# Performance work log

Measured on AMD Instinct MI355X. Metric: run time of the kernel, lower is better.

Reference implementation:

```python
import jax, jax.numpy as jnp
import numpy as np

# --- static configuration (matches init_kwargs / input_specs) ---
B, QB, D, NH, HD = 4, 512, 256, 8, 32   # batch, queries/batch, d_model, heads, head_dim
HALF = HD // 2                            # rotation pairs per head
L = 4                                     # n_levels
SIZES = [3, 5, 7, 9]                      # neighborhood size per level
K = sum(s * s for s in SIZES)             # 164 keys per query
SHAPES = np.array([[8, 8], [16, 16], [32, 32], [64, 64]], dtype=np.int32)
HMAX = 64                                 # finest-level spatial extent
LN_EPS = 1e-5
ROPE_THETA = 10.0


def make_rope_freqs():
    # Grouped-frequency ND RoPE: spatial dims (i, j) in freq group 0 (theta=10),
    # level dim in group 1 (theta = rope_theta/100 = 0.1). HALF slots split:
    # group0 -> HALF/2 (HALF/4 per spatial dim), group1 -> HALF/2.
    n_sp = HALF // 4   # 4 slots for i, 4 for j
    n_lv = HALF // 2   # 8 slots for level
    f = np.zeros((3, HALF), np.float32)
    f_sp = ROPE_THETA ** (-np.arange(n_sp, dtype=np.float32) / n_sp)
    f_lv = (ROPE_THETA / 100.0) ** (-np.arange(n_lv, dtype=np.float32) / n_lv)
    f[0, 0:n_sp] = f_sp
    f[1, n_sp:2 * n_sp] = f_sp
    f[2, 2 * n_sp:] = f_lv
    return jnp.asarray(np.tile(f[None], (NH, 1, 1)))  # [NH, 3, HALF]


def neighborhood_indices(qpos, shapes):
    # qpos: [N,4] float (b, i, j, level); queries live at the finest level so
    # (i, j) are full-scale coords. Returns (b,i,j,l) int indices [N,K,4] and
    # full-scale key positions (i_full, j_full, level) [N,K,3].
    N = qpos.shape[0]
    b = qpos[:, 0].astype(jnp.int32)
    q_ij = qpos[:, 1:3]
    shapes_f = shapes.astype(jnp.float32)
    scal = shapes_f / shapes_f[-1]  # [L,2]: H_l / H_finest
    idx_parts, pos_parts = [], []
    for m, size in enumerate(SIZES):
        center = jnp.floor(q_ij * scal[m]).astype(jnp.int32)  # [N,2] at level m
        r = jnp.arange(size, dtype=jnp.int32) - (size - 1) // 2
        off = jnp.stack(jnp.meshgrid(r, r, indexing='ij'), -1).reshape(-1, 2)
        nb = center[:, None, :] + off[None]                    # [N, s*s, 2]
        lev_i = jnp.full((N, size * size, 1), m, jnp.int32)
        idx_parts.append(jnp.concatenate([nb, lev_i], -1))
        pos_parts.append(jnp.concatenate(
            [nb.astype(jnp.float32) / scal[m],                 # back to full scale
             jnp.full((N, size * size, 1), float(m))], -1))
    ijl = jnp.concatenate(idx_parts, 1)       # [N,K,3]
    key_pos = jnp.concatenate(pos_parts, 1)   # [N,K,3]
    bijl = jnp.concatenate([jnp.broadcast_to(b[:, None, None], (N, K, 1)), ijl], -1)
    return bijl, key_pos


def gather_values(fmap, bijl, shapes):
    # fmap: dense stand-in for the sparse COO pyramid, [B, HMAX, HMAX, L, D];
    # level l only occupies the top-left [H_l, W_l] block -> out-of-range keys
    # are "unspecified" (value 0, masked out of the softmax).
    b, i, j, l = bijl[..., 0], bijl[..., 1], bijl[..., 2], bijl[..., 3]
    hw = shapes[l]  # [N,K,2]
    valid = (i >= 0) & (i < hw[..., 0]) & (j >= 0) & (j < hw[..., 1])
    ic = jnp.clip(i, 0, HMAX - 1)
    jc = jnp.clip(j, 0, HMAX - 1)
    val = fmap[b, ic, jc, l]  # [N,K,D]
    return val * valid[..., None], valid


def layer_norm(x, g, b_):
    mu = x.mean(-1, keepdims=True)
    var = ((x - mu) ** 2).mean(-1, keepdims=True)
    return (x - mu) * jax.lax.rsqrt(var + LN_EPS) * g + b_


def apply_rope(x, pos, freqs):
    # x: [..., NH, HD], pos: [..., 3], freqs: [NH, 3, HALF]
    ang = jnp.einsum('...p,hpf->...hf', pos, freqs)
    c, s = jnp.cos(ang), jnp.sin(ang)
    xr = x.reshape(x.shape[:-1] + (HALF, 2))
    x1, x2 = xr[..., 0], xr[..., 1]
    return jnp.stack([x1 * c - x2 * s, x1 * s + x2 * c], -1).reshape(x.shape)


def setup_inputs() -> dict:
    key = jax.random.key(0)
    ks = jax.random.split(key, 8)
    N = B * QB
    q_ij = jax.random.uniform(ks[0], (N, 2), minval=0.5, maxval=float(HMAX) - 0.5)
    batch = jnp.repeat(jnp.arange(B, dtype=jnp.float32), QB)
    lev = jnp.full((N, 1), float(L - 1))  # all queries at the finest level
    query_positions_bijl = jnp.concatenate([batch[:, None], q_ij, lev], -1)
    sc = D ** -0.5
    return {
        'query': jax.random.normal(ks[1], (N, D), jnp.float32),
        'query_positions_bijl': query_positions_bijl,
        'query_batch_offsets': jnp.arange(B + 1, dtype=jnp.int32) * QB,
        'stacked_feature_maps': jax.random.normal(ks[2], (B, HMAX, HMAX, L, D), jnp.float32),
        'level_spatial_shapes': jnp.asarray(SHAPES),
        'ln_gamma': jnp.ones((D,), jnp.float32),
        'ln_beta': jnp.zeros((D,), jnp.float32),
        'Wq': jax.random.normal(ks[3], (D, D), jnp.float32) * sc,
        'Wkv': jax.random.normal(ks[4], (D, 2 * D), jnp.float32) * sc,
        'Wout': jax.random.normal(ks[5], (D, D), jnp.float32) * sc,
        'rope_freqs': make_rope_freqs(),
    }


def reference(query, query_positions_bijl, query_batch_offsets, stacked_feature_maps,
              level_spatial_shapes, ln_gamma, ln_beta, Wq, Wkv, Wout, rope_freqs):
    N = query.shape[0]
    bijl, key_pos = neighborhood_indices(query_positions_bijl, level_spatial_shapes)
    value, specified = gather_values(stacked_feature_maps, bijl, level_spatial_shapes)
    residual = query
    qn = layer_norm(query, ln_gamma, ln_beta)  # norm_first
    q = qn @ Wq                                # [N, D]
    kv = value @ Wkv                           # [N, K, 2D]
    k, v = jnp.split(kv, 2, axis=-1)
    q = apply_rope(q.reshape(B, QB, NH, HD),
                   query_positions_bijl[:, 1:].reshape(B, QB, 3), rope_freqs)
    k = apply_rope(k.reshape(B, QB, K, NH, HD),
                   key_pos.reshape(B, QB, K, 3), rope_freqs)
    v = v.reshape(B, QB, K, NH, HD)
    # NOTE: original module applies no 1/sqrt(head_dim) scaling -- kept faithful.
    scores = jnp.einsum('bqhd,bqkhd->bhqk', q, k)
    mask = specified.reshape(B, QB, K)[:, None]  # [B,1,QB,K]
    scores = jnp.where(mask, scores, -jnp.inf)
    w = jax.nn.softmax(scores, axis=-1)
    x = jnp.einsum('bhqk,bqkhd->bqhd', w, v)
    x = x.reshape(N, D) @ Wout
    return x + residual
```

## Files before the change

### kernel.cpp

```cpp
#include <hip/hip_runtime.h>
#include <math.h>

#define NQ    2048
#define Dd    256
#define NHh   8
#define HDd   32
#define KK    164
#define KP    192
#define PPB   5440
#define M_TOT 21760
#define TWO_D 512

using bf16x8  = __attribute__((ext_vector_type(8))) short;
using f32x4   = __attribute__((ext_vector_type(4))) float;
using ushort8 = __attribute__((ext_vector_type(8))) unsigned short;

__device__ __forceinline__ unsigned short bf16_rne(float x) {
    unsigned u = __float_as_uint(x);
    return (unsigned short)((u + 0x7fffu + ((u >> 16) & 1u)) >> 16);
}
__device__ __forceinline__ float bf2f(unsigned short h) {
    return __uint_as_float((unsigned)h << 16);
}

__device__ __forceinline__ void gload_lds16(const void* g, void* s) {
    __builtin_amdgcn_global_load_lds(
        (const __attribute__((address_space(1))) void*)g,
        (__attribute__((address_space(3))) void*)s, 16, 0, 0);
}

__device__ __forceinline__ void row_geom(int r, int& l, int& S, int& base, int& lg, int& inv) {
    if      (r < 64)   { l = 0; S = 8;  base = 0;    lg = 3; inv = 8; }
    else if (r < 320)  { l = 1; S = 16; base = 64;   lg = 4; inv = 4; }
    else if (r < 1344) { l = 2; S = 32; base = 320;  lg = 5; inv = 2; }
    else               { l = 3; S = 64; base = 1344; lg = 6; inv = 1; }
}

__device__ __forceinline__ void split_one(const float* __restrict__ W,
                                          unsigned short* __restrict__ hi_,
                                          unsigned short* __restrict__ lo_,
                                          int N, int gid) {
    int k = gid & 255, n = gid >> 8;
    float x = W[k * N + n];
    unsigned short h = bf16_rne(x);
    hi_[n * 256 + k] = h;
    lo_[n * 256 + k] = bf16_rne(x - bf2f(h));
}

__global__ __launch_bounds__(256) void prep(const float* __restrict__ fmap,
                                            const float* __restrict__ Wkv,
                                            const float* __restrict__ Wq,
                                            const float* __restrict__ Wout,
                                            const float* __restrict__ query,
                                            const float* __restrict__ gamma,
                                            const float* __restrict__ beta,
                                            unsigned short* __restrict__ Ahi,
                                            unsigned short* __restrict__ Alo,
                                            unsigned short* __restrict__ WkvThi,
                                            unsigned short* __restrict__ WkvTlo,
                                            unsigned short* __restrict__ WqThi,
                                            unsigned short* __restrict__ WqTlo,
                                            unsigned short* __restrict__ WoThi,
                                            unsigned short* __restrict__ WoTlo,
                                            unsigned short* __restrict__ Xhi,
                                            unsigned short* __restrict__ Xlo) {
    __shared__ float red[4];
    const int bid = blockIdx.x, t = threadIdx.x;

    if (bid < 5440) {
        int gid = bid * 256 + t;
        int m = gid >> 6, c4 = (gid & 63) << 2;
        int b = m / PPB, r = m - b * PPB;
        int l, S, base, lg, inv;
        row_geom(r, l, S, base, lg, inv);
        int idx = r - base;
        int i = idx >> lg, j = idx & (S - 1);
        size_t rowOff = ((size_t)((b * 64 + i) * 64 + j)) * 1024 + l * 256;
        const float4 v = *(const float4*)(fmap + rowOff + c4);
        ushort4 hi, lo;
        hi.x = bf16_rne(v.x); lo.x = bf16_rne(v.x - bf2f(hi.x));
        hi.y = bf16_rne(v.y); lo.y = bf16_rne(v.y - bf2f(hi.y));
        hi.z = bf16_rne(v.z); lo.z = bf16_rne(v.z - bf2f(hi.z));
        hi.w = bf16_rne(v.w); lo.w = bf16_rne(v.w - bf2f(hi.w));
        *(ushort4*)(Ahi + (size_t)m * 256 + c4) = hi;
        *(ushort4*)(Alo + (size_t)m * 256 + c4) = lo;
    } else if (bid < 5952) {
        split_one(Wkv, WkvThi, WkvTlo, 512, (bid - 5440) * 256 + t);
    } else if (bid < 6208) {
        split_one(Wq, WqThi, WqTlo, 256, (bid - 5952) * 256 + t);
    } else if (bid < 6464) {
        split_one(Wout, WoThi, WoTlo, 256, (bid - 6208) * 256 + t);
    } else {
        const int q = bid - 6464, wid = t >> 6;
        float x = query[q * Dd + t];
        float s = x;
#pragma unroll
        for (int mK = 32; mK >= 1; mK >>= 1) s += __shfl_xor(s, mK);
        if ((t & 63) == 0) red[wid] = s;
        __syncthreads();
        float mu = (red[0] + red[1] + red[2] + red[3]) * (1.0f / 256.0f);
        float dx = x - mu;
        float s2 = dx * dx;
#pragma unroll
        for (int mK = 32; mK >= 1; mK >>= 1) s2 += __shfl_xor(s2, mK);
        __syncthreads();
        if ((t & 63) == 0) red[wid] = s2;
        __syncthreads();
        float var = (red[0] + red[1] + red[2] + red[3]) * (1.0f / 256.0f);
        float v = dx * rsqrtf(var + 1e-5f) * gamma[t] + beta[t];
        unsigned short hi = bf16_rne(v);
        Xhi[q * Dd + t] = hi;
        Xlo[q * Dd + t] = bf16_rne(v - bf2f(hi));
    }
}

__global__ __launch_bounds__(256) void kv_gemm_mfma(const unsigned short* __restrict__ Ahi,
                                                    const unsigned short* __restrict__ Alo,
                                                    const unsigned short* __restrict__ Bthi,
                                                    const unsigned short* __restrict__ Btlo,
                                                    const float* __restrict__ freqs,
                                                    unsigned short* __restrict__ kv16) {
    __shared__ __align__(16) short As[2][2][128 * 32];
    __shared__ __align__(16) short Bs[2][2][128 * 32];

    const int bid = blockIdx.x;
    const int my = (bid >> 5) * 8 + (bid & 7);
    const int mx = (bid >> 3) & 3;
    if (my >= 170) return;

    const int t  = threadIdx.x;
    const int w  = t >> 6, l = t & 63;
    const int wr = w >> 1, wc = w & 1;
    const int n0 = mx * 128, bm = my * 128;
    const int lr = l & 15, ks = l >> 4;
    const int ksw8 = ((ks ^ ((lr >> 1) & 3)) << 3);
    const bool doRope = (n0 < 256);

    f32x4 acc[4][4];
#pragma unroll
    for (int i = 0; i < 4; i++)
#pragma unroll
        for (int j = 0; j < 4; j++) { f32x4 z = {0.f,0.f,0.f,0.f}; acc[i][j] = z; }

    const int srow = l >> 2, sslot = l & 3;
    const int gs = sslot ^ ((srow >> 1) & 3);

    auto stage = [&](int kt, int buf) {
        size_t k0b = (size_t)(kt << 6);
#pragma unroll
        for (int i = 0; i < 2; i++) {
            int rb = w * 32 + i * 16;
            int m  = rb + srow;
            size_t aofs = (((size_t)(bm + m)) << 9) + k0b + (gs << 4);
            size_t bofs = (((size_t)(n0 + m)) << 9) + k0b + (gs << 4);
            gload_lds16((const char*)Ahi  + aofs, (void*)&As[buf][0][rb * 32]);
            gload_lds16((const char*)Alo  + aofs, (void*)&As[buf][1][rb * 32]);
            gload_lds16((const char*)Bthi + bofs, (void*)&Bs[buf][0][rb * 32]);
            gload_lds16((const char*)Btlo + bofs, (void*)&Bs[buf][1][rb * 32]);
        }
    };

    stage(0, 0);
    __syncthreads();

    for (int kt = 0; kt < 8; kt++) {
        int cur = kt & 1;
        if (kt < 7) stage(kt + 1, cur ^ 1);

        bf16x8 aH[4], aL[4], bH[4], bL[4];
#pragma unroll
        for (int f = 0; f < 4; f++) {
            int m = wr * 64 + f * 16 + lr;
            aH[f] = *(const bf16x8*)&As[cur][0][m * 32 + ksw8];
            aL[f] = *(const bf16x8*)&As[cur][1][m * 32 + ksw8];
            int n = wc * 64 + f * 16 + lr;
            bH[f] = *(const bf16x8*)&Bs[cur][0][n * 32 + ksw8];
            bL[f] = *(const bf16x8*)&Bs[cur][1][n * 32 + ksw8];
        }
#pragma unroll
        for (int i = 0; i < 4; i++)
#pragma unroll
            for (int j = 0; j < 4; j++)
                acc[i][j] = __builtin_amdgcn_mfma_f32_16x16x32_bf16(aH[i], bH[j],
                                                                    acc[i][j], 0, 0, 0);
#pragma unroll
        for (int i = 0; i < 4; i++)
#pragma unroll
            for (int j = 0; j < 4; j++)
                acc[i][j] = __builtin_amdgcn_mfma_f32_16x16x32_bf16(aH[i], bL[j],
                                                                    acc[i][j], 0, 0, 0);
#pragma unroll
        for (int i = 0; i < 4; i++)
#pragma unroll
            for (int j = 0; j < 4; j++)
                acc[i][j] = __builtin_amdgcn_mfma_f32_16x16x32_bf16(aL[i], bH[j],
                                                                    acc[i][j], 0, 0, 0);
        __syncthreads();
    }

    float fx0 = 0.f, fy0 = 0.f, fz0 = 0.f, fx1 = 0.f, fy1 = 0.f, fz1 = 0.f;
    if (doRope) {
        int e0 = lr >> 1, e1 = e0 + 8;
        fx0 = freqs[e0]; fy0 = freqs[16 + e0]; fz0 = freqs[32 + e0];
        fx1 = freqs[e1]; fy1 = freqs[16 + e1]; fz1 = freqs[32 + e1];
    }
#pragma unroll
    for (int i = 0; i < 4; i++) {
        int mg = bm + wr * 64 + i * 16 + ks * 4;
#pragma unroll
        for (int r = 0; r < 4; r++) {
            int m = mg + r;
            float c0 = 1.f, s0 = 0.f, c1 = 1.f, s1 = 0.f;
            if (doRope) {
                int b = m / PPB;
                int rw = m - b * PPB;
                int lL, S, base, lg, inv;
                row_geom(rw, lL, S, base, lg, inv);
                int idx = rw - base;
                float px = (float)((idx >> lg) * inv);
                float py = (float)((idx & (S - 1)) * inv);
                float pl = (float)lL;
                __sincosf(px * fx0 + py * fy0 + pl * fz0, &s0, &c0);
                __sincosf(px * fx1 + py * fy1 + pl * fz1, &s1, &c1);
            }
#pragma unroll
            for (int j = 0; j < 4; j++) {
                int ng = n0 + wc * 64 + j * 16 + lr;
                float self = acc[i][j][r];
                float part = __shfl_xor(self, 1);
                if (!(lr & 1)) {
                    float y1 = self, y2 = part;
                    if (doRope) {
                        float c = (j & 1) ? c1 : c0;
                        float s = (j & 1) ? s1 : s0;
                        y1 = self * c - part * s;
                        y2 = self * s + part * c;
                    }
                    unsigned word = (unsigned)bf16_rne(y1) | ((unsigned)bf16_rne(y2) << 16);
                    *(unsigned*)(kv16 + (size_t)m * TWO_D + ng) = word;
                }
            }
        }
    }
}

template<bool RESID>
__global__ __launch_bounds__(256) void proj_gemm(const unsigned short* __restrict__ Ahi,
                                                 const unsigned short* __restrict__ Alo,
                                                 const unsigned short* __restrict__ Bthi,
                                                 const unsigned short* __restrict__ Btlo,
                                                 float* __restrict__ C,
                                                 const float* __restrict__ resid) {
    __shared__ __align__(16) short As[2][2][64 * 32];
    __shared__ __align__(16) short Bs[2][2][32 * 32];

    const int t  = threadIdx.x;
    const int w  = t >> 6, l = t & 63;
    const int n0 = blockIdx.x * 32, bm = blockIdx.y * 64;
    const int lr = l & 15, ks = l >> 4;
    const int ksw8 = ((ks ^ ((lr >> 1) & 3)) << 3);

    f32x4 acc[2];
#pragma unroll
    for (int j = 0; j < 2; j++) { f32x4 z = {0.f,0.f,0.f,0.f}; acc[j] = z; }

    const int srow = l >> 2, sslot = l & 3;
    const int gs = sslot ^ ((srow >> 1) & 3);

    auto stage = [&](int kt, int buf) {
        size_t k0b = (size_t)(kt << 6);
        {
            int rb = w * 16;
            int m  = rb + srow;
            size_t aofs = (((size_t)(bm + m)) << 9) + k0b + (gs << 4);
            gload_lds16((const char*)Ahi + aofs, (void*)&As[buf][0][rb * 32]);
            gload_lds16((const char*)Alo + aofs, (void*)&As[buf][1][rb * 32]);
        }
        {
            int sel = w >> 1;
            int rb  = (w & 1) * 16;
            int m   = rb + srow;
            const unsigned short* Bp = sel ? Btlo : Bthi;
            size_t bofs = (((size_t)(n0 + m)) << 9) + k0b + (gs << 4);
            gload_lds16((const char*)Bp + bofs, (void*)&Bs[buf][sel][rb * 32]);
        }
    };

    stage(0, 0);
    __syncthreads();

    for (int kt = 0; kt < 8; kt++) {
        int cur = kt & 1;
        if (kt < 7) stage(kt + 1, cur ^ 1);

        bf16x8 aH, aL, bH[2], bL[2];
        {
            int m = w * 16 + lr;
            aH = *(const bf16x8*)&As[cur][0][m * 32 + ksw8];
            aL = *(const bf16x8*)&As[cur][1][m * 32 + ksw8];
        }
#pragma unroll
        for (int j = 0; j < 2; j++) {
            int n = j * 16 + lr;
            bH[j] = *(const bf16x8*)&Bs[cur][0][n * 32 + ksw8];
            bL[j] = *(const bf16x8*)&Bs[cur][1][n * 32 + ksw8];
        }
#pragma unroll
        for (int j = 0; j < 2; j++)
            acc[j] = __builtin_amdgcn_mfma_f32_16x16x32_bf16(aH, bH[j], acc[j], 0, 0, 0);
#pragma unroll
        for (int j = 0; j < 2; j++)
            acc[j] = __builtin_amdgcn_mfma_f32_16x16x32_bf16(aH, bL[j], acc[j], 0, 0, 0);
#pragma unroll
        for (int j = 0; j < 2; j++)
            acc[j] = __builtin_amdgcn_mfma_f32_16x16x32_bf16(aL, bH[j], acc[j], 0, 0, 0);
        __syncthreads();
    }

    {
        int mg = bm + w * 16 + ks * 4;
#pragma unroll
        for (int j = 0; j < 2; j++) {
            int ng = n0 + j * 16 + lr;
#pragma unroll
            for (int r = 0; r < 4; r++) {
                float v = acc[j][r];
                if (RESID) v += resid[(size_t)(mg + r) * 256 + ng];
                C[(size_t)(mg + r) * 256 + ng] = v;
            }
        }
    }
}

__global__ __launch_bounds__(256) void attn_core(const float* __restrict__ qr,
                                                 const float* __restrict__ qpos,
                                                 const unsigned short* __restrict__ kv16,
                                                 const float* __restrict__ freqs,
                                                 unsigned short* __restrict__ Phi,
                                                 unsigned short* __restrict__ Plo) {
    __shared__ __align__(16) float qsh[Dd];
    __shared__ float sL[NHh * KP];
    __shared__ int   kidx[KP];
    __shared__ float attnP[8][Dd];
    __shared__ float invS[NHh];

    const int q = ((blockIdx.x & 7) << 8) | (blockIdx.x >> 3);
    const int t = threadIdx.x;
    const int h = t >> 5, lane = t & 31;

    float qx = qpos[q * 4 + 1];
    float qy = qpos[q * 4 + 2];
    int   bb = (int)qpos[q * 4 + 0];

    {
        float x = qr[q * Dd + t];
        int f = (t & 31) >> 1;
        float ang = qx * freqs[f] + qy * freqs[16 + f] + 3.0f * freqs[32 + f];
        float c = cosf(ang), sn = sinf(ang);
        float partner = __shfl_xor(x, 1);
        qsh[t] = (!(t & 1)) ? (x * c - partner * sn) : (partner * sn + x * c);
    }

    if (t < KP) {
        int k = t;
        int kv = -1;
        if (k < KK) {
            int S, base, off, sz, half, lg;
            if      (k < 9)  { S = 8;  base = 0;    off = k;      sz = 3; half = 1; lg = 3; }
            else if (k < 34) { S = 16; base = 64;   off = k - 9;  sz = 5; half = 2; lg = 4; }
            else if (k < 83) { S = 32; base = 320;  off = k - 34; sz = 7; half = 3; lg = 5; }
            else             { S = 64; base = 1344; off = k - 83; sz = 9; half = 4; lg = 6; }
            int di = off / sz - half;
            int dj = off % sz - half;
            float scal = (float)S * (1.0f / 64.0f);
            int ci = (int)floorf(qx * scal);
            int cj = (int)floorf(qy * scal);
            int i = ci + di, j = cj + dj;
            bool valid = (i >= 0) & (i < S) & (j >= 0) & (j < S);
            kv = valid ? (bb * PPB + base + (i << lg) + j) : -1;
        }
        kidx[t] = kv;
    }
    __syncthreads();

    float qreg[32];
#pragma unroll
    for (int i = 0; i < 32; i++) qreg[i] = qsh[h * HDd + i];

#pragma unroll
    for (int ct = 0; ct < 6; ++ct) {
        int k = ct * 32 + lane;
        int ki = kidx[k];
        int kr = ki < 0 ? 0 : ki;
        const ushort8* kp = (const ushort8*)(kv16 + (size_t)kr * TWO_D + h * HDd);
        float c0 = 0.f, c1 = 0.f;
#pragma unroll
        for (int s4 = 0; s4 < 4; s4++) {
            ushort8 kvv = kp[s4];
            float* cc = (s4 & 1) ? &c1 : &c0;
#pragma unroll
            for (int e = 0; e < 8; e++)
                *cc = fmaf(qreg[s4 * 8 + e], bf2f(kvv[e]), *cc);
        }
        sL[h * KP + k] = (ki >= 0) ? (c0 + c1) : -INFINITY;
    }
    __syncthreads();

    float mx = -INFINITY;
#pragma unroll
    for (int ct = 0; ct < 6; ++ct) mx = fmaxf(mx, sL[h * KP + ct * 32 + lane]);
#pragma unroll
    for (int mK = 16; mK >= 1; mK >>= 1) mx = fmaxf(mx, __shfl_xor(mx, mK));
    float se = 0.f;
#pragma unroll
    for (int ct = 0; ct < 6; ++ct) {
        int k = ct * 32 + lane;
        float e = __expf(sL[h * KP + k] - mx);
        sL[h * KP + k] = e;
        se += e;
    }
#pragma unroll
    for (int mK = 16; mK >= 1; mK >>= 1) se += __shfl_xor(se, mK);
    if (lane == 0) invS[h] = 1.0f / se;
    __syncthreads();

    {
        const int rep  = t >> 6;
        const int half = (t >> 5) & 1;
        const int l5   = t & 31;
        const int hh   = l5 >> 2;
        const int oct  = l5 & 3;
        float a[8];
#pragma unroll
        for (int e = 0; e < 8; e++) a[e] = 0.f;
        const unsigned short* vbase = kv16 + Dd + hh * HDd + oct * 8;
#pragma unroll 4
        for (int it = 0; it < 24; it++) {
            int k = rep * 48 + it * 2 + half;
            float w0 = sL[hh * KP + k];
            int kr = kidx[k]; kr = kr < 0 ? 0 : kr;
            ushort8 vv = *(const ushort8*)(vbase + (size_t)kr * TWO_D);
#pragma unroll
            for (int e = 0; e < 8; e++) a[e] = fmaf(w0, bf2f(vv[e]), a[e]);
        }
        float* dst = &attnP[t >> 5][hh * HDd + oct * 8];
#pragma unroll
        for (int e = 0; e < 8; e++) dst[e] = a[e];
    }
    __syncthreads();

    float val = 0.f;
#pragma unroll
    for (int s = 0; s < 8; s++) val += attnP[s][t];
    val *= invS[h];
    unsigned short hi = bf16_rne(val);
    Phi[q * Dd + t] = hi;
    Plo[q * Dd + t] = bf16_rne(val - bf2f(hi));
}

#define BMf 128
#define BNf 128
#define KTf 16

__global__ __launch_bounds__(256) void kv_gemm(const float* __restrict__ fmap,
                                               const float* __restrict__ Wkv,
                                               float* __restrict__ kvws) {
    __shared__ float Asf[KTf][BMf + 4];
    __shared__ float Bsf[KTf][BNf + 4];
    __shared__ int   rowOff[BMf];

    const int t  = threadIdx.x;
    const int bm = blockIdx.x * BMf;
    const int n0 = blockIdx.y * BNf;

    if (t < BMf) {
        int m = bm + t;
        int b = m / PPB;
        int r = m - b * PPB;
        int l, S, base, lg, inv;
        row_geom(r, l, S, base, lg, inv);
        int idx = r - base;
        int i = idx >> lg;
        int j = idx & (S - 1);
        rowOff[t] = ((b * 64 + i) * 64 + j) * 1024 + l * 256;
    }
    __syncthreads();

    const int tx = t & 15, ty = t >> 4;
    float acc[8][8];
#pragma unroll
    for (int i = 0; i < 8; i++)
#pragma unroll
        for (int j = 0; j < 8; j++) acc[i][j] = 0.f;

    for (int k0 = 0; k0 < Dd; k0 += KTf) {
#pragma unroll
        for (int s = 0; s < 2; s++) {
            int task = t + s * 256;
            int row  = task >> 2;
            int k4   = (task & 3) * 4;
            const float4 v = *(const float4*)(fmap + rowOff[row] + k0 + k4);
            Asf[k4 + 0][row] = v.x;
            Asf[k4 + 1][row] = v.y;
            Asf[k4 + 2][row] = v.z;
            Asf[k4 + 3][row] = v.w;
        }
#pragma unroll
        for (int s = 0; s < 2; s++) {
            int task = t + s * 256;
            int kk   = task >> 5;
            int c4   = (task & 31) * 4;
            *(float4*)(&Bsf[kk][c4]) = *(const float4*)(Wkv + (k0 + kk) * TWO_D + n0 + c4);
        }
        __syncthreads();
#pragma unroll
        for (int kk = 0; kk < KTf; kk++) {
            float a[8], bb[8];
#pragma unroll
            for (int i = 0; i < 8; i++) a[i]  = Asf[kk][ty * 8 + i];
#pragma unroll
            for (int j = 0; j < 8; j++) bb[j] = Bsf[kk][tx * 8 + j];
#pragma unroll
            for (int i = 0; i < 8; i++)
#pragma unroll
                for (int j = 0; j < 8; j++)
                    acc[i][j] = fmaf(a[i], bb[j], acc[i][j]);
        }
        __syncthreads();
    }

#pragma unroll
    for (int i = 0; i < 8; i++) {
        int m = bm + ty * 8 + i;
        float* dst = kvws + (size_t)m * TWO_D + n0 + tx * 8;
#pragma unroll
        for (int j = 0; j < 8; j += 4) {
            *(float4*)(dst + j) = make_float4(acc[i][j], acc[i][j + 1],
                                              acc[i][j + 2], acc[i][j + 3]);
        }
    }
}

__global__ __launch_bounds__(256) void rope_k_f32(float* __restrict__ kvws,
                                                  const float* __restrict__ freqs) {
    int gid = blockIdx.x * 256 + threadIdx.x;
    int m = gid >> 7;
    int p = gid & 127;
    int f = p & 15;
    int b = m / PPB;
    int r = m - b * PPB;
    int l, S, base, lg, inv;
    row_geom(r, l, S, base, lg, inv);
    int idx = r - base;
    int i = idx >> lg;
    int j = idx & (S - 1);
    float px = (float)(i * inv), py = (float)(j * inv), pl = (float)l;
    float ang = px * freqs[f] + py * freqs[16 + f] + pl * freqs[32 + f];
    float c = cosf(ang), s = sinf(ang);
    float2* kp = (float2*)kvws + (size_t)m * 256 + p;
    float2 v = *kp;
    *kp = make_float2(v.x * c - v.y * s, v.x * s + v.y * c);
}

__global__ __launch_bounds__(256) void attn_fused(const float* __restrict__ query,
                                                  const float* __restrict__ qpos,
                                                  const float* __restrict__ Wq,
                                                  const float* __restrict__ Wout,
                                                  const float* __restrict__ gamma,
                                                  const float* __restrict__ beta,
                                                  const float* __restrict__ freqs,
                                                  const float* __restrict__ kvws,
                                                  float* __restrict__ out) {
    __shared__ float qn[Dd];
    __shared__ __align__(16) float qsh[Dd];
    __shared__ float sL[NHh * KK];
    __shared__ int   kidx[KK];
    __shared__ float attnL[Dd];
    __shared__ float red[4];
    __shared__ float invS[NHh];

    const int q = blockIdx.x;
    const int t = threadIdx.x;
    const int wid = t >> 6;
    const int h = t >> 5, lane = t & 31;

    float x = query[q * Dd + t];
    float s = x;
#pragma unroll
    for (int mK = 32; mK >= 1; mK >>= 1) s += __shfl_xor(s, mK);
    if ((t & 63) == 0) red[wid] = s;
    __syncthreads();
    float mu = (red[0] + red[1] + red[2] + red[3]) * (1.0f / 256.0f);
    float dx = x - mu;
    float s2 = dx * dx;
#pragma unroll
    for (int mK = 32; mK >= 1; mK >>= 1) s2 += __shfl_xor(s2, mK);
    __syncthreads();
    if ((t & 63) == 0) red[wid] = s2;
    __syncthreads();
    float var = (red[0] + red[1] + red[2] + red[3]) * (1.0f / 256.0f);
    float rs = rsqrtf(var + 1e-5f);
    qn[t] = dx * rs * gamma[t] + beta[t];
    __syncthreads();

    float a0 = 0.f, a1 = 0.f, a2 = 0.f, a3 = 0.f;
#pragma unroll 8
    for (int d = 0; d < Dd; d += 4) {
        a0 = fmaf(qn[d + 0], Wq[(d + 0) * Dd + t], a0);
        a1 = fmaf(qn[d + 1], Wq[(d + 1) * Dd + t], a1);
        a2 = fmaf(qn[d + 2], Wq[(d + 2) * Dd + t], a2);
        a3 = fmaf(qn[d + 3], Wq[(d + 3) * Dd + t], a3);
    }
    float acc = (a0 + a1) + (a2 + a3);

    float qx = qpos[q * 4 + 1];
    float qy = qpos[q * 4 + 2];
    int   bb = (int)qpos[q * 4 + 0];
    {
        int f = (t & 31) >> 1;
        float ang = qx * freqs[f] + qy * freqs[16 + f] + 3.0f * freqs[32 + f];
        float c = cosf(ang), sn = sinf(ang);
        float partner = __shfl_xor(acc, 1);
        bool ev = !(t & 1);
        acc = ev ? (acc * c - partner * sn) : (partner * sn + acc * c);
    }
    qsh[t] = acc;

    if (t < KK) {
        int k = t;
        int S, base, off, sz, half, lg;
        if      (k < 9)  { S = 8;  base = 0;    off = k;      sz = 3; half = 1; lg = 3; }
        else if (k < 34) { S = 16; base = 64;   off = k - 9;  sz = 5; half = 2; lg = 4; }
        else if (k < 83) { S = 32; base = 320;  off = k - 34; sz = 7; half = 3; lg = 5; }
        else             { S = 64; base = 1344; off = k - 83; sz = 9; half = 4; lg = 6; }
        int di = off / sz - half;
        int dj = off % sz - half;
        float scal = (float)S * (1.0f / 64.0f);
        int ci = (int)floorf(qx * scal);
        int cj = (int)floorf(qy * scal);
        int i = ci + di, j = cj + dj;
        bool valid = (i >= 0) & (i < S) & (j >= 0) & (j < S);
        kidx[t] = valid ? (bb * PPB + base + (i << lg) + j) : -1;
    }
    __syncthreads();

    float4 qv[8];
    {
        const float4* qp = (const float4*)(qsh + h * HDd);
#pragma unroll
        for (int i = 0; i < 8; i++) qv[i] = qp[i];
    }
#pragma unroll
    for (int ct = 0; ct < 6; ++ct) {
        int k = ct * 32 + lane;
        if (k >= KK) break;
        int ki = kidx[k];
        int kr = ki < 0 ? 0 : ki;
        const float4* kp = (const float4*)(kvws + (size_t)kr * TWO_D + h * HDd);
        float c0 = 0.f, c1 = 0.f;
#pragma unroll
        for (int i = 0; i < 8; i += 2) {
            float4 k0v = kp[i], k1v = kp[i + 1];
            c0 = fmaf(qv[i].x, k0v.x, c0); c0 = fmaf(qv[i].y, k0v.y, c0);
            c0 = fmaf(qv[i].z, k0v.z, c0); c0 = fmaf(qv[i].w, k0v.w, c0);
            c1 = fmaf(qv[i + 1].x, k1v.x, c1); c1 = fmaf(qv[i + 1].y, k1v.y, c1);
            c1 = fmaf(qv[i + 1].z, k1v.z, c1); c1 = fmaf(qv[i + 1].w, k1v.w, c1);
        }
        sL[h * KK + k] = (ki >= 0) ? (c0 + c1) : -INFINITY;
    }
    __syncthreads();

    float mx = -INFINITY;
    for (int k = lane; k < KK; k += 32) mx = fmaxf(mx, sL[h * KK + k]);
#pragma unroll
    for (int mK = 16; mK >= 1; mK >>= 1) mx = fmaxf(mx, __shfl_xor(mx, mK));
    float se = 0.f;
    for (int k = lane; k < KK; k += 32) {
        float e = expf(sL[h * KK + k] - mx);
        sL[h * KK + k] = e;
        se += e;
    }
#pragma unroll
    for (int mK = 16; mK >= 1; mK >>= 1) se += __shfl_xor(se, mK);
    if (lane == 0) invS[h] = 1.0f / se;
    __syncthreads();

    float p0 = 0.f, p1 = 0.f, p2 = 0.f, p3 = 0.f;
#pragma unroll 4
    for (int k = 0; k < 164; k += 4) {
        int ki0 = kidx[k],     kr0 = ki0 < 0 ? 0 : ki0;
        int ki1 = kidx[k + 1], kr1 = ki1 < 0 ? 0 : ki1;
        int ki2 = kidx[k + 2], kr2 = ki2 < 0 ? 0 : ki2;
        int ki3 = kidx[k + 3], kr3 = ki3 < 0 ? 0 : ki3;
        p0 = fmaf(sL[h * KK + k],     kvws[(size_t)kr0 * TWO_D + Dd + t], p0);
        p1 = fmaf(sL[h * KK + k + 1], kvws[(size_t)kr1 * TWO_D + Dd + t], p1);
        p2 = fmaf(sL[h * KK + k + 2], kvws[(size_t)kr2 * TWO_D + Dd + t], p2);
        p3 = fmaf(sL[h * KK + k + 3], kvws[(size_t)kr3 * TWO_D + Dd + t], p3);
    }
    attnL[t] = ((p0 + p1) + (p2 + p3)) * invS[h];
    __syncthreads();

    float o0 = query[q * Dd + t], o1 = 0.f, o2 = 0.f, o3 = 0.f;
#pragma unroll 8
    for (int d = 0; d < Dd; d += 4) {
        o0 = fmaf(attnL[d + 0], Wout[(d + 0) * Dd + t], o0);
        o1 = fmaf(attnL[d + 1], Wout[(d + 1) * Dd + t], o1);
        o2 = fmaf(attnL[d + 2], Wout[(d + 2) * Dd + t], o2);
        o3 = fmaf(attnL[d + 3], Wout[(d + 3) * Dd + t], o3);
    }
    out[q * Dd + t] = (o0 + o1) + (o2 + o3);
}

extern "C" void kernel_launch(void* const* d_in, const int* in_sizes, int n_in,
                              void* d_out, int out_size, void* d_ws, size_t ws_size,
                              hipStream_t stream) {
    const float* query = (const float*)d_in[0];
    const float* qpos  = (const float*)d_in[1];
    const float* fmap  = (const float*)d_in[3];
    const float* gamma = (const float*)d_in[5];
    const float* beta  = (const float*)d_in[6];
    const float* Wq    = (const float*)d_in[7];
    const float* Wkv   = (const float*)d_in[8];
    const float* Wout  = (const float*)d_in[9];
    const float* freqs = (const float*)d_in[10];
    float* out = (float*)d_out;

    const size_t O_KV16   = 0;
    const size_t O_AHI    = 22282240;
    const size_t O_ALO    = 33423360;
    const size_t O_WKVHI  = 44564480;
    const size_t O_WKVLO  = 44826624;
    const size_t O_WQHI   = 45088768;
    const size_t O_WQLO   = 45219840;
    const size_t O_WOHI   = 45350912;
    const size_t O_WOLO   = 45481984;
    const size_t O_XHI    = 45613056;
    const size_t O_XLO    = 46661632;
    const size_t O_QR     = 47710208;
    const size_t O_PHI    = 49807360;
    const size_t O_PLO    = 50855936;
    const size_t need     = 51904512;

    if (ws_size >= need) {
        char* base = (char*)d_ws;
        unsigned short* kv16   = (unsigned short*)(base + O_KV16);
        unsigned short* Ahi    = (unsigned short*)(base + O_AHI);
        unsigned short* Alo    = (unsigned short*)(base + O_ALO);
        unsigned short* WkvThi = (unsigned short*)(base + O_WKVHI);
        unsigned short* WkvTlo = (unsigned short*)(base + O_WKVLO);
        unsigned short* WqThi  = (unsigned short*)(base + O_WQHI);
        unsigned short* WqTlo  = (unsigned short*)(base + O_WQLO);
        unsigned short* WoThi  = (unsigned short*)(base + O_WOHI);
        unsigned short* WoTlo  = (unsigned short*)(base + O_WOLO);
        unsigned short* Xhi    = (unsigned short*)(base + O_XHI);
        unsigned short* Xlo    = (unsigned short*)(base + O_XLO);
        float*          qrw    = (float*)        (base + O_QR);
        unsigned short* Phi    = (unsigned short*)(base + O_PHI);
        unsigned short* Plo    = (unsigned short*)(base + O_PLO);

        prep<<<dim3(8512), 256, 0, stream>>>(fmap, Wkv, Wq, Wout, query, gamma, beta,
                                             Ahi, Alo, WkvThi, WkvTlo,
                                             WqThi, WqTlo, WoThi, WoTlo, Xhi, Xlo);
        kv_gemm_mfma<<<dim3(704), 256, 0, stream>>>(Ahi, Alo, WkvThi, WkvTlo,
                                                    freqs, kv16);
        proj_gemm<false><<<dim3(8, 32), 256, 0, stream>>>(Xhi, Xlo, WqThi, WqTlo,
                                                          qrw, nullptr);
        attn_core<<<dim3(NQ), 256, 0, stream>>>(qrw, qpos, kv16, freqs, Phi, Plo);
        proj_gemm<true><<<dim3(8, 32), 256, 0, stream>>>(Phi, Plo, WoThi, WoTlo,
                                                         out, query);
    } else {
        float* kvws = (float*)d_ws;
        kv_gemm<<<dim3(M_TOT / BMf, TWO_D / BNf), 256, 0, stream>>>(fmap, Wkv, kvws);
        rope_k_f32<<<dim3((M_TOT * 128) / 256), 256, 0, stream>>>(kvws, freqs);
        attn_fused<<<dim3(NQ), 256, 0, stream>>>(query, qpos, Wq, Wout, gamma, beta,
                                                 freqs, kvws, out);
    }
}
```

Baseline: 197.8 us.

## Fuse feature-map gather and bf16 split into KV GEMM, merge Q projection launch

The KV GEMM now reads fp32 feature-map rows straight from the gathered positions and splits them into bf16 hi/lo inside its staging step. This removes the separate prep pass that wrote the hi/lo A matrices to workspace and read them back. The Q projection GEMM is folded into the same launch as extra blocks, which saves one kernel launch. The cost is that A staging now goes through registers instead of async global-to-LDS loads, so it may overlap less with the MFMA work.

Measured after the change: 192.8 us. 1.03x faster.

```diff
diff --git a/kernel.cpp b/kernel.cpp
--- a/kernel.cpp
+++ b/kernel.cpp
@@ -36,6 +36,17 @@
     else               { l = 3; S = 64; base = 1344; lg = 6; inv = 1; }
 }
 
+__device__ __forceinline__ void split8(const float4& a, const float4& b,
+                                       ushort8& hi, ushort8& lo) {
+    float x[8] = {a.x, a.y, a.z, a.w, b.x, b.y, b.z, b.w};
+#pragma unroll
+    for (int e = 0; e < 8; e++) {
+        unsigned short h = bf16_rne(x[e]);
+        hi[e] = h;
+        lo[e] = bf16_rne(x[e] - bf2f(h));
+    }
+}
+
 __device__ __forceinline__ void split_one(const float* __restrict__ W,
                                           unsigned short* __restrict__ hi_,
                                           unsigned short* __restrict__ lo_,
@@ -47,15 +58,12 @@
     lo_[n * 256 + k] = bf16_rne(x - bf2f(h));
 }
 
-__global__ __launch_bounds__(256) void prep(const float* __restrict__ fmap,
-                                            const float* __restrict__ Wkv,
+__global__ __launch_bounds__(256) void prep(const float* __restrict__ Wkv,
                                             const float* __restrict__ Wq,
                                             const float* __restrict__ Wout,
                                             const float* __restrict__ query,
                                             const float* __restrict__ gamma,
                                             const float* __restrict__ beta,
-                                            unsigned short* __restrict__ Ahi,
-                                            unsigned short* __restrict__ Alo,
                                             unsigned short* __restrict__ WkvThi,
                                             unsigned short* __restrict__ WkvTlo,
                                             unsigned short* __restrict__ WqThi,
@@ -67,31 +75,14 @@
     __shared__ float red[4];
     const int bid = blockIdx.x, t = threadIdx.x;
 
-    if (bid < 5440) {
-        int gid = bid * 256 + t;
-        int m = gid >> 6, c4 = (gid & 63) << 2;
-        int b = m / PPB, r = m - b * PPB;
-        int l, S, base, lg, inv;
-        row_geom(r, l, S, base, lg, inv);
-        int idx = r - base;
-        int i = idx >> lg, j = idx & (S - 1);
-        size_t rowOff = ((size_t)((b * 64 + i) * 64 + j)) * 1024 + l * 256;
-        const float4 v = *(const float4*)(fmap + rowOff + c4);
-        ushort4 hi, lo;
-        hi.x = bf16_rne(v.x); lo.x = bf16_rne(v.x - bf2f(hi.x));
-        hi.y = bf16_rne(v.y); lo.y = bf16_rne(v.y - bf2f(hi.y));
-        hi.z = bf16_rne(v.z); lo.z = bf16_rne(v.z - bf2f(hi.z));
-        hi.w = bf16_rne(v.w); lo.w = bf16_rne(v.w - bf2f(hi.w));
-        *(ushort4*)(Ahi + (size_t)m * 256 + c4) = hi;
-        *(ushort4*)(Alo + (size_t)m * 256 + c4) = lo;
-    } else if (bid < 5952) {
-        split_one(Wkv, WkvThi, WkvTlo, 512, (bid - 5440) * 256 + t);
-    } else if (bid < 6208) {
-        split_one(Wq, WqThi, WqTlo, 256, (bid - 5952) * 256 + t);
-    } else if (bid < 6464) {
-        split_one(Wout, WoThi, WoTlo, 256, (bid - 6208) * 256 + t);
+    if (bid < 512) {
+        split_one(Wkv, WkvThi, WkvTlo, 512, bid * 256 + t);
+    } else if (bid < 768) {
+        split_one(Wq, WqThi, WqTlo, 256, (bid - 512) * 256 + t);
+    } else if (bid < 1024) {
+        split_one(Wout, WoThi, WoTlo, 256, (bid - 768) * 256 + t);
     } else {
-        const int q = bid - 6464, wid = t >> 6;
+        const int q = bid - 1024, wid = t >> 6;
         float x = query[q * Dd + t];
         float s = x;
 #pragma unroll
@@ -114,143 +105,257 @@
     }
 }
 
-__global__ __launch_bounds__(256) void kv_gemm_mfma(const unsigned short* __restrict__ Ahi,
-                                                    const unsigned short* __restrict__ Alo,
-                                                    const unsigned short* __restrict__ Bthi,
-                                                    const unsigned short* __restrict__ Btlo,
-                                                    const float* __restrict__ freqs,
-                                                    unsigned short* __restrict__ kv16) {
-    __shared__ __align__(16) short As[2][2][128 * 32];
-    __shared__ __align__(16) short Bs[2][2][128 * 32];
+__global__ __launch_bounds__(256) void kvq_gemm(const float* __restrict__ fmap,
+                                                const unsigned short* __restrict__ Bthi,
+                                                const unsigned short* __restrict__ Btlo,
+                                                const unsigned short* __restrict__ Xhi,
+                                                const unsigned short* __restrict__ Xlo,
+                                                const unsigned short* __restrict__ WqThi,
+                                                const unsigned short* __restrict__ WqTlo,
+                                                const float* __restrict__ freqs,
+                                                unsigned short* __restrict__ kv16,
+                                                float* __restrict__ qrw) {
+    __shared__ __align__(16) char smem[66048];
 
     const int bid = blockIdx.x;
-    const int my = (bid >> 5) * 8 + (bid & 7);
-    const int mx = (bid >> 3) & 3;
-    if (my >= 170) return;
-
-    const int t  = threadIdx.x;
-    const int w  = t >> 6, l = t & 63;
-    const int wr = w >> 1, wc = w & 1;
-    const int n0 = mx * 128, bm = my * 128;
+    const int t = threadIdx.x;
+    const int w = t >> 6, l = t & 63;
     const int lr = l & 15, ks = l >> 4;
     const int ksw8 = ((ks ^ ((lr >> 1) & 3)) << 3);
-    const bool doRope = (n0 < 256);
-
-    f32x4 acc[4][4];
-#pragma unroll
-    for (int i = 0; i < 4; i++)
-#pragma unroll
-        for (int j = 0; j < 4; j++) { f32x4 z = {0.f,0.f,0.f,0.f}; acc[i][j] = z; }
-
     const int srow = l >> 2, sslot = l & 3;
     const int gs = sslot ^ ((srow >> 1) & 3);
 
-    auto stage = [&](int kt, int buf) {
-        size_t k0b = (size_t)(kt << 6);
-#pragma unroll
-        for (int i = 0; i < 2; i++) {
-            int rb = w * 32 + i * 16;
-            int m  = rb + srow;
-            size_t aofs = (((size_t)(bm + m)) << 9) + k0b + (gs << 4);
-            size_t bofs = (((size_t)(n0 + m)) << 9) + k0b + (gs << 4);
-            gload_lds16((const char*)Ahi  + aofs, (void*)&As[buf][0][rb * 32]);
-            gload_lds16((const char*)Alo  + aofs, (void*)&As[buf][1][rb * 32]);
-            gload_lds16((const char*)Bthi + bofs, (void*)&Bs[buf][0][rb * 32]);
-            gload_lds16((const char*)Btlo + bofs, (void*)&Bs[buf][1][rb * 32]);
-        }
-    };
-
-    stage(0, 0);
-    __syncthreads();
-
-    for (int kt = 0; kt < 8; kt++) {
-        int cur = kt & 1;
-        if (kt < 7) stage(kt + 1, cur ^ 1);
-
-        bf16x8 aH[4], aL[4], bH[4], bL[4];
-#pragma unroll
-        for (int f = 0; f < 4; f++) {
-            int m = wr * 64 + f * 16 + lr;
-            aH[f] = *(const bf16x8*)&As[cur][0][m * 32 + ksw8];
-            aL[f] = *(const bf16x8*)&As[cur][1][m * 32 + ksw8];
-            int n = wc * 64 + f * 16 + lr;
-            bH[f] = *(const bf16x8*)&Bs[cur][0][n * 32 + ksw8];
-            bL[f] = *(const bf16x8*)&Bs[cur][1][n * 32 + ksw8];
-        }
+    if (bid < 704) {
+        const int my = (bid >> 5) * 8 + (bid & 7);
+        const int mx = (bid >> 3) & 3;
+        if (my >= 170) return;
+
+        const int wr = w >> 1, wc = w & 1;
+        const int n0 = mx * 128, bm = my * 128;
+        const bool doRope = (n0 < 256);
+
+        short* AsB = (short*)smem;
+        short* BsB = (short*)(smem + 32768);
+        int*   rofs = (int*)(smem + 65536);
+        auto ASP = [&](int buf, int sel) { return AsB + (buf * 2 + sel) * 4096; };
+        auto BSP = [&](int buf, int sel) { return BsB + (buf * 2 + sel) * 4096; };
+
+        if (t < 128) {
+            int m = bm + t;
+            int b = m / PPB, r = m - b * PPB;
+            int lL, S, base, lg, inv;
+            row_geom(r, lL, S, base, lg, inv);
+            int idx = r - base;
+            rofs[t] = ((b * 64 + (idx >> lg)) * 64 + (idx & (S - 1))) * 1024 + lL * 256;
+        }
+        __syncthreads();
+
+        f32x4 acc[4][4];
 #pragma unroll
         for (int i = 0; i < 4; i++)
 #pragma unroll
-            for (int j = 0; j < 4; j++)
-                acc[i][j] = __builtin_amdgcn_mfma_f32_16x16x32_bf16(aH[i], bH[j],
-                                                                    acc[i][j], 0, 0, 0);
-#pragma unroll
-        for (int i = 0; i < 4; i++)
-#pragma unroll
-            for (int j = 0; j < 4; j++)
-                acc[i][j] = __builtin_amdgcn_mfma_f32_16x16x32_bf16(aH[i], bL[j],
-                                                                    acc[i][j], 0, 0, 0);
-#pragma unroll
-        for (int i = 0; i < 4; i++)
-#pragma unroll
-            for (int j = 0; j < 4; j++)
-                acc[i][j] = __builtin_amdgcn_mfma_f32_16x16x32_bf16(aL[i], bH[j],
-                                                                    acc[i][j], 0, 0, 0);
+            for (int j = 0; j < 4; j++) { f32x4 z = {0.f,0.f,0.f,0.f}; acc[i][j] = z; }
+
+        auto stageA = [&](int kt, int buf) {
+            const int row = t >> 1;
+            const int kh  = (t & 1) << 4;
+            const float* src = fmap + rofs[row] + (kt << 5) + kh;
+            float4 v0 = *(const float4*)(src);
+            float4 v1 = *(const float4*)(src + 4);
+            float4 v2 = *(const float4*)(src + 8);
+            float4 v3 = *(const float4*)(src + 12);
+            ushort8 h0, l0, h1, l1;
+            split8(v0, v1, h0, l0);
+            split8(v2, v3, h1, l1);
+            const int sw = (row >> 1) & 3;
+            const int s0 = kh >> 3;
+            short* ah = ASP(buf, 0) + row * 32;
+            short* al = ASP(buf, 1) + row * 32;
+            *(ushort8*)(ah + ((s0 ^ sw) << 3))       = h0;
+            *(ushort8*)(ah + (((s0 + 1) ^ sw) << 3)) = h1;
+            *(ushort8*)(al + ((s0 ^ sw) << 3))       = l0;
+            *(ushort8*)(al + (((s0 + 1) ^ sw) << 3)) = l1;
+        };
+        auto stageB = [&](int kt, int buf) {
+            size_t k0b = (size_t)(kt << 6);
+#pragma unroll
+            for (int i = 0; i < 2; i++) {
+                int rb = w * 32 + i * 16;
+                int m  = rb + srow;
+                size_t bofs = (((size_t)(n0 + m)) << 9) + k0b + (gs << 4);
+                gload_lds16((const char*)Bthi + bofs, (void*)(BSP(buf, 0) + rb * 32));
+                gload_lds16((const char*)Btlo + bofs, (void*)(BSP(buf, 1) + rb * 32));
+            }
+        };
+
+        stageA(0, 0);
+        stageB(0, 0);
         __syncthreads();
-    }
-
-    float fx0 = 0.f, fy0 = 0.f, fz0 = 0.f, fx1 = 0.f, fy1 = 0.f, fz1 = 0.f;
-    if (doRope) {
-        int e0 = lr >> 1, e1 = e0 + 8;
-        fx0 = freqs[e0]; fy0 = freqs[16 + e0]; fz0 = freqs[32 + e0];
-        fx1 = freqs[e1]; fy1 = freqs[16 + e1]; fz1 = freqs[32 + e1];
-    }
-#pragma unroll
-    for (int i = 0; i < 4; i++) {
-        int mg = bm + wr * 64 + i * 16 + ks * 4;
-#pragma unroll
-        for (int r = 0; r < 4; r++) {
-            int m = mg + r;
-            float c0 = 1.f, s0 = 0.f, c1 = 1.f, s1 = 0.f;
-            if (doRope) {
-                int b = m / PPB;
-                int rw = m - b * PPB;
-                int lL, S, base, lg, inv;
-                row_geom(rw, lL, S, base, lg, inv);
-                int idx = rw - base;
-                float px = (float)((idx >> lg) * inv);
-                float py = (float)((idx & (S - 1)) * inv);
-                float pl = (float)lL;
-                __sincosf(px * fx0 + py * fy0 + pl * fz0, &s0, &c0);
-                __sincosf(px * fx1 + py * fy1 + pl * fz1, &s1, &c1);
+
+        for (int kt = 0; kt < 8; kt++) {
+            int cur = kt & 1;
+            if (kt < 7) {
+                stageA(kt + 1, cur ^ 1);
+                stageB(kt + 1, cur ^ 1);
             }
-#pragma unroll
-            for (int j = 0; j < 4; j++) {
-                int ng = n0 + wc * 64 + j * 16 + lr;
-                float self = acc[i][j][r];
-                float part = __shfl_xor(self, 1);
-                if (!(lr & 1)) {
-                    float y1 = self, y2 = part;
-                    if (doRope) {
-                        float c = (j & 1) ? c1 : c0;
-                        float s = (j & 1) ? s1 : s0;
-                        y1 = self * c - part * s;
-                        y2 = self * s + part * c;
+
+            bf16x8 aH[4], aL[4], bH[4], bL[4];
+#pragma unroll
+            for (int f = 0; f < 4; f++) {
+                int m = wr * 64 + f * 16 + lr;
+                aH[f] = *(const bf16x8*)(ASP(cur, 0) + m * 32 + ksw8);
+                aL[f] = *(const bf16x8*)(ASP(cur, 1) + m * 32 + ksw8);
+                int n = wc * 64 + f * 16 + lr;
+                bH[f] = *(const bf16x8*)(BSP(cur, 0) + n * 32 + ksw8);
+                bL[f] = *(const bf16x8*)(BSP(cur, 1) + n * 32 + ksw8);
+            }
+#pragma unroll
+            for (int i = 0; i < 4; i++)
+#pragma unroll
+                for (int j = 0; j < 4; j++)
+                    acc[i][j] = __builtin_amdgcn_mfma_f32_16x16x32_bf16(aH[i], bH[j],
+                                                                        acc[i][j], 0, 0, 0);
+#pragma unroll
+            for (int i = 0; i < 4; i++)
+#pragma unroll
+                for (int j = 0; j < 4; j++)
+                    acc[i][j] = __builtin_amdgcn_mfma_f32_16x16x32_bf16(aH[i], bL[j],
+                                                                        acc[i][j], 0, 0, 0);
+#pragma unroll
+            for (int i = 0; i < 4; i++)
+#pragma unroll
+                for (int j = 0; j < 4; j++)
+                    acc[i][j] = __builtin_amdgcn_mfma_f32_16x16x32_bf16(aL[i], bH[j],
+                                                                        acc[i][j], 0, 0, 0);
+            __syncthreads();
+        }
+
+        float fx0 = 0.f, fy0 = 0.f, fz0 = 0.f, fx1 = 0.f, fy1 = 0.f, fz1 = 0.f;
+        if (doRope) {
+            int e0 = lr >> 1, e1 = e0 + 8;
+            fx0 = freqs[e0]; fy0 = freqs[16 + e0]; fz0 = freqs[32 + e0];
+            fx1 = freqs[e1]; fy1 = freqs[16 + e1]; fz1 = freqs[32 + e1];
+        }
+#pragma unroll
+        for (int i = 0; i < 4; i++) {
+            int mg = bm + wr * 64 + i * 16 + ks * 4;
+#pragma unroll
+            for (int r = 0; r < 4; r++) {
+                int m = mg + r;
+                float c0 = 1.f, s0 = 0.f, c1 = 1.f, s1 = 0.f;
+                if (doRope) {
+                    int b = m / PPB;
+                    int rw = m - b * PPB;
+                    int lL, S, base, lg, inv;
+                    row_geom(rw, lL, S, base, lg, inv);
+                    int idx = rw - base;
+                    float px = (float)((idx >> lg) * inv);
+                    float py = (float)((idx & (S - 1)) * inv);
+                    float pl = (float)lL;
+                    __sincosf(px * fx0 + py * fy0 + pl * fz0, &s0, &c0);
+                    __sincosf(px * fx1 + py * fy1 + pl * fz1, &s1, &c1);
+                }
+#pragma unroll
+                for (int j = 0; j < 4; j++) {
+                    int ng = n0 + wc * 64 + j * 16 + lr;
+                    float self = acc[i][j][r];
+                    float part = __shfl_xor(self, 1);
+                    if (!(lr & 1)) {
+                        float y1 = self, y2 = part;
+                        if (doRope) {
+                            float c = (j & 1) ? c1 : c0;
+                            float s = (j & 1) ? s1 : s0;
+                            y1 = self * c - part * s;
+                            y2 = self * s + part * c;
+                        }
+                        unsigned word = (unsigned)bf16_rne(y1) | ((unsigned)bf16_rne(y2) << 16);
+                        *(unsigned*)(kv16 + (size_t)m * TWO_D + ng) = word;
                     }
-                    unsigned word = (unsigned)bf16_rne(y1) | ((unsigned)bf16_rne(y2) << 16);
-                    *(unsigned*)(kv16 + (size_t)m * TWO_D + ng) = word;
                 }
             }
         }
-    }
-}
-
-template<bool RESID>
-__global__ __launch_bounds__(256) void proj_gemm(const unsigned short* __restrict__ Ahi,
-                                                 const unsigned short* __restrict__ Alo,
-                                                 const unsigned short* __restrict__ Bthi,
-                                                 const unsigned short* __restrict__ Btlo,
-                                                 float* __restrict__ C,
-                                                 const float* __restrict__ resid) {
+    } else {
+        const int pbid = bid - 704;
+        const int n0 = (pbid & 7) * 32, bm = (pbid >> 3) * 64;
+
+        short* AsB = (short*)smem;
+        short* BsB = (short*)(smem + 16384);
+        auto ASQ = [&](int buf, int sel) { return AsB + (buf * 2 + sel) * 2048; };
+        auto BSQ = [&](int buf, int sel) { return BsB + (buf * 2 + sel) * 1024; };
+
+        f32x4 acc[2];
+#pragma unroll
+        for (int j = 0; j < 2; j++) { f32x4 z = {0.f,0.f,0.f,0.f}; acc[j] = z; }
+
+        auto stage = [&](int kt, int buf) {
+            size_t k0b = (size_t)(kt << 6);
+            {
+                int rb = w * 16;
+                int m  = rb + srow;
+                size_t aofs = (((size_t)(bm + m)) << 9) + k0b + (gs << 4);
+                gload_lds16((const char*)Xhi + aofs, (void*)(ASQ(buf, 0) + rb * 32));
+                gload_lds16((const char*)Xlo + aofs, (void*)(ASQ(buf, 1) + rb * 32));
+            }
+            {
+                int sel = w >> 1;
+                int rb  = (w & 1) * 16;
+                int m   = rb + srow;
+                const unsigned short* Bp = sel ? WqTlo : WqThi;
+                size_t bofs = (((size_t)(n0 + m)) << 9) + k0b + (gs << 4);
+                gload_lds16((const char*)Bp + bofs, (void*)(BSQ(buf, sel) + rb * 32));
+            }
+        };
+
+        stage(0, 0);
+        __syncthreads();
+
+        for (int kt = 0; kt < 8; kt++) {
+            int cur = kt & 1;
+            if (kt < 7) stage(kt + 1, cur ^ 1);
+
+            bf16x8 aH, aL, bH[2], bL[2];
+            {
+                int m = w * 16 + lr;
+                aH = *(const bf16x8*)(ASQ(cur, 0) + m * 32 + ksw8);
+                aL = *(const bf16x8*)(ASQ(cur, 1) + m * 32 + ksw8);
+            }
+#pragma unroll
+            for (int j = 0; j < 2; j++) {
+                int n = j * 16 + lr;
+                bH[j] = *(const bf16x8*)(BSQ(cur, 0) + n * 32 + ksw8);
+                bL[j] = *(const bf16x8*)(BSQ(cur, 1) + n * 32 + ksw8);
+            }
+#pragma unroll
+            for (int j = 0; j < 2; j++)
+                acc[j] = __builtin_amdgcn_mfma_f32_16x16x32_bf16(aH, bH[j], acc[j], 0, 0, 0);
+#pragma unroll
+            for (int j = 0; j < 2; j++)
+                acc[j] = __builtin_amdgcn_mfma_f32_16x16x32_bf16(aH, bL[j], acc[j], 0, 0, 0);
+#pragma unroll
+            for (int j = 0; j < 2; j++)
+                acc[j] = __builtin_amdgcn_mfma_f32_16x16x32_bf16(aL, bH[j], acc[j], 0, 0, 0);
+            __syncthreads();
+        }
+
+        {
+            int mg = bm + w * 16 + ks * 4;
+#pragma unroll
+            for (int j = 0; j < 2; j++) {
+                int ng = n0 + j * 16 + lr;
+#pragma unroll
+                for (int r = 0; r < 4; r++)
+                    qrw[(size_t)(mg + r) * 256 + ng] = acc[j][r];
+            }
+        }
+    }
+}
+
+__global__ __launch_bounds__(256) void proj_out(const unsigned short* __restrict__ Ahi,
+                                                const unsigned short* __restrict__ Alo,
+                                                const unsigned short* __restrict__ Bthi,
+                                                const unsigned short* __restrict__ Btlo,
+                                                float* __restrict__ C,
+                                                const float* __restrict__ resid) {
     __shared__ __align__(16) short As[2][2][64 * 32];
     __shared__ __align__(16) short Bs[2][2][32 * 32];
 
@@ -323,11 +428,8 @@
         for (int j = 0; j < 2; j++) {
             int ng = n0 + j * 16 + lr;
 #pragma unroll
-            for (int r = 0; r < 4; r++) {
-                float v = acc[j][r];
-                if (RESID) v += resid[(size_t)(mg + r) * 256 + ng];
-                C[(size_t)(mg + r) * 256 + ng] = v;
-            }
+            for (int r = 0; r < 4; r++)
+                C[(size_t)(mg + r) * 256 + ng] = acc[j][r] + resid[(size_t)(mg + r) * 256 + ng];
         }
     }
 }
@@ -726,8 +828,6 @@
     float* out = (float*)d_out;
 
     const size_t O_KV16   = 0;
-    const size_t O_AHI    = 22282240;
-    const size_t O_ALO    = 33423360;
     const size_t O_WKVHI  = 44564480;
     const size_t O_WKVLO  = 44826624;
     const size_t O_WQHI   = 45088768;
@@ -744,8 +844,6 @@
     if (ws_size >= need) {
         char* base = (char*)d_ws;
         unsigned short* kv16   = (unsigned short*)(base + O_KV16);
-        unsigned short* Ahi    = (unsigned short*)(base + O_AHI);
-        unsigned short* Alo    = (unsigned short*)(base + O_ALO);
         unsigned short* WkvThi = (unsigned short*)(base + O_WKVHI);
         unsigned short* WkvTlo = (unsigned short*)(base + O_WKVLO);
         unsigned short* WqThi  = (unsigned short*)(base + O_WQHI);
@@ -758,16 +856,15 @@
         unsigned short* Phi    = (unsigned short*)(base + O_PHI);
         unsigned short* Plo    = (unsigned short*)(base + O_PLO);
 
-        prep<<<dim3(8512), 256, 0, stream>>>(fmap, Wkv, Wq, Wout, query, gamma, beta,
-                                             Ahi, Alo, WkvThi, WkvTlo,
-                                             WqThi, WqTlo, WoThi, WoTlo, Xhi, Xlo);
-        kv_gemm_mfma<<<dim3(704), 256, 0, stream>>>(Ahi, Alo, WkvThi, WkvTlo,
-                                                    freqs, kv16);
-        proj_gemm<false><<<dim3(8, 32), 256, 0, stream>>>(Xhi, Xlo, WqThi, WqTlo,
-                                                          qrw, nullptr);
+        prep<<<dim3(3072), 256, 0, stream>>>(Wkv, Wq, Wout, query, gamma, beta,
+                                             WkvThi, WkvTlo, WqThi, WqTlo,
+                                             WoThi, WoTlo, Xhi, Xlo);
+        kvq_gemm<<<dim3(960), 256, 0, stream>>>(fmap, WkvThi, WkvTlo,
+                                                Xhi, Xlo, WqThi, WqTlo,
+                                                freqs, kv16, qrw);
         attn_core<<<dim3(NQ), 256, 0, stream>>>(qrw, qpos, kv16, freqs, Phi, Plo);
-        proj_gemm<true><<<dim3(8, 32), 256, 0, stream>>>(Phi, Plo, WoThi, WoTlo,
-                                                         out, query);
+        proj_out<<<dim3(8, 32), 256, 0, stream>>>(Phi, Plo, WoThi, WoTlo,
+                                                  out, query);
     } else {
         float* kvws = (float*)d_ws;
         kv_gemm<<<dim3(M_TOT / BMf, TWO_D / BNf), 256, 0, stream>>>(fmap, Wkv, kvws);
```
